# Kernel optimization log

Measured on AMD Instinct MI355X. Metric: run time of the kernel, lower is better.

Reference implementation:

```python
import jax, jax.numpy as jnp
import numpy as np

D_MODEL = 1024
H = 16
D_K = D_MODEL // H


def setup_inputs() -> dict:
    key = jax.random.key(0)
    ks = jax.random.split(key, 10)
    B, S = 2, 2048
    s = 1.0 / np.sqrt(D_MODEL)
    x = jax.random.normal(ks[0], (B, S, D_MODEL), dtype=jnp.float32)
    mask = jax.random.randint(ks[1], (B, 1, S, S), 0, 2, dtype=jnp.int32)
    w_q = jax.random.normal(ks[2], (D_MODEL, D_MODEL), dtype=jnp.float32) * s
    b_q = jnp.zeros((D_MODEL,), dtype=jnp.float32)
    w_k = jax.random.normal(ks[3], (D_MODEL, D_MODEL), dtype=jnp.float32) * s
    b_k = jnp.zeros((D_MODEL,), dtype=jnp.float32)
    w_v = jax.random.normal(ks[4], (D_MODEL, D_MODEL), dtype=jnp.float32) * s
    b_v = jnp.zeros((D_MODEL,), dtype=jnp.float32)
    w_o = jax.random.normal(ks[5], (D_MODEL, D_MODEL), dtype=jnp.float32) * s
    b_o = jnp.zeros((D_MODEL,), dtype=jnp.float32)
    return {"x": x, "mask": mask, "w_q": w_q, "b_q": b_q, "w_k": w_k,
            "b_k": b_k, "w_v": w_v, "b_v": b_v, "w_o": w_o, "b_o": b_o}


def reference(x, mask, w_q, b_q, w_k, b_k, w_v, b_v, w_o, b_o):
    B, S, _ = x.shape
    # projections; weights stored as (in, out) equivalents of torch Linear
    q = (x @ w_q + b_q).reshape(B, S, H, D_K).transpose(0, 2, 1, 3)  # bhsd
    k = (x @ w_k + b_k).reshape(B, S, H, D_K).transpose(0, 2, 1, 3)
    v = (x @ w_v + b_v).reshape(B, S, H, D_K).transpose(0, 2, 1, 3)
    scores = jnp.einsum('bhqd,bhkd->bhqk', q, k) / jnp.sqrt(jnp.float32(D_K))
    scores = jnp.where(mask == 0, jnp.float32(-1e9), scores)
    attn = jax.nn.softmax(scores, axis=-1)  # dropout omitted (eval mode)
    out = jnp.einsum('bhqk,bhkd->bhqd', attn, v)
    out = out.transpose(0, 2, 1, 3).reshape(B, S, D_MODEL)
    return out @ w_o + b_o
```

## Files before the change

### kernel.cpp

```cpp
#include <hip/hip_runtime.h>
#include <hip/hip_bf16.h>
#include <stdint.h>

#define D_MODEL 1024
#define NH 16
#define DK 64
#define SEQ 2048
#define BATCH 2
#define NTOK (BATCH * SEQ)

typedef __bf16 bf16;
typedef float f32x4 __attribute__((ext_vector_type(4)));
typedef __bf16 bf16x8 __attribute__((ext_vector_type(8)));
typedef __bf16 bf16x4 __attribute__((ext_vector_type(4)));

#define QSCALE 0.18033687932432668f

__device__ __forceinline__ void gload_lds16(const void* g, void* l) {
  __builtin_amdgcn_global_load_lds(
      (const __attribute__((address_space(1))) void*)g,
      (__attribute__((address_space(3))) void*)l, 16, 0, 0);
}

__global__ void prep_kernel(const float* __restrict__ x, bf16* __restrict__ xb,
                            const float* __restrict__ wq, const float* __restrict__ wk,
                            const float* __restrict__ wv, const float* __restrict__ wo,
                            bf16* __restrict__ wt,
                            const int* __restrict__ mask, unsigned long long* __restrict__ bits) {
  __shared__ float tile[32][33];
  const int bx = blockIdx.x;
  const int tid = threadIdx.x;
  if (bx < 4096) {
    int i = bx * 256 + tid;
    float4 v = reinterpret_cast<const float4*>(x)[i];
    bf16x4 o;
    o[0] = (bf16)v.x; o[1] = (bf16)v.y; o[2] = (bf16)v.z; o[3] = (bf16)v.w;
    reinterpret_cast<bf16x4*>(xb)[i] = o;
  } else if (bx < 8192) {
    int blk = bx - 4096;
    const int jt = blk & 127;
    const int kt = blk >> 7;
    const int tx = tid & 31, ty = tid >> 5;
    const int j0 = jt * 32;
    const int sel = j0 >> 10;
    const float* w = (sel == 0) ? wq : (sel == 1) ? wk : (sel == 2) ? wv : wo;
    const int jj0 = j0 & 1023;
#pragma unroll
    for (int i = 0; i < 4; ++i)
      tile[ty + i * 8][tx] = w[(size_t)(kt * 32 + ty + i * 8) * 1024 + jj0 + tx];
    __syncthreads();
#pragma unroll
    for (int i = 0; i < 4; ++i)
      wt[(size_t)(j0 + ty + i * 8) * 1024 + kt * 32 + tx] = (bf16)tile[tx][ty + i * 8];
  } else {
    int gt = (bx - 8192) * 256 + tid;
    int wid = gt >> 6;
    int l = gt & 63;
    int m = mask[(size_t)wid * 64 + l];
    unsigned long long b = __ballot(m != 0);
    if (l == 0) bits[wid] = b;
  }
}

__global__ __launch_bounds__(256) void gemm_qkv(
    const bf16* __restrict__ A, const bf16* __restrict__ Bt,
    const float* __restrict__ b0, const float* __restrict__ b1, const float* __restrict__ b2,
    bf16* __restrict__ out_q, bf16* __restrict__ out_k, bf16* __restrict__ out_vt) {
  __shared__ __align__(16) bf16 As[128 * 32];
  __shared__ __align__(16) bf16 Bs[128 * 32];
  const int tid = threadIdx.x;
  const int w = tid >> 6, l = tid & 63;
  const int wr = w >> 1, wc = w & 1;
  const int m0 = blockIdx.y * 128, n0 = blockIdx.x * 128;
  f32x4 acc[4][4] = {};
  const int lrow = l >> 2;
  const int lc8 = (l & 3) * 8;
  char* AsB = (char*)As;
  char* BsB = (char*)Bs;

  for (int k0 = 0; k0 < 1024; k0 += 32) {
#pragma unroll
    for (int is = 0; is < 2; ++is) {
      int arow = m0 + is * 64 + w * 16 + lrow;
      gload_lds16(A + (size_t)arow * 1024 + k0 + lc8, AsB + is * 4096 + w * 1024);
      int brow = n0 + is * 64 + w * 16 + lrow;
      gload_lds16(Bt + (size_t)brow * 1024 + k0 + lc8, BsB + is * 4096 + w * 1024);
    }
    __syncthreads();
    bf16x8 af[4], bfr[4];
#pragma unroll
    for (int m = 0; m < 4; ++m)
      af[m] = *reinterpret_cast<const bf16x8*>(As + (wr * 64 + m * 16 + (l & 15)) * 32 + (l >> 4) * 8);
#pragma unroll
    for (int n = 0; n < 4; ++n)
      bfr[n] = *reinterpret_cast<const bf16x8*>(Bs + (wc * 64 + n * 16 + (l & 15)) * 32 + (l >> 4) * 8);
#pragma unroll
    for (int m = 0; m < 4; ++m)
#pragma unroll
      for (int n = 0; n < 4; ++n)
        acc[m][n] = __builtin_amdgcn_mfma_f32_16x16x32_bf16(af[m], bfr[n], acc[m][n], 0, 0, 0);
    __syncthreads();
  }

#pragma unroll
  for (int m = 0; m < 4; ++m) {
    int ib = m0 + wr * 64 + m * 16 + 4 * (l >> 4);
#pragma unroll
    for (int n = 0; n < 4; ++n) {
      int j = n0 + wc * 64 + n * 16 + (l & 15);
      int sel = j >> 10, jj = j & 1023;
      const float* bp = (sel == 0) ? b0 : (sel == 1) ? b1 : b2;
      float bias = bp[jj];
      if (sel == 0) {
#pragma unroll
        for (int r = 0; r < 4; ++r)
          out_q[(size_t)(ib + r) * 1024 + jj] = (bf16)((acc[m][n][r] + bias) * QSCALE);
      } else if (sel == 1) {
#pragma unroll
        for (int r = 0; r < 4; ++r)
          out_k[(size_t)(ib + r) * 1024 + jj] = (bf16)(acc[m][n][r] + bias);
      } else {
        int hh = jj >> 6, dd = jj & 63;
        int bb = ib >> 11, ss = ib & 2047;
        bf16x4 v;
#pragma unroll
        for (int r = 0; r < 4; ++r) v[r] = (bf16)(acc[m][n][r] + bias);
        *reinterpret_cast<bf16x4*>(out_vt + ((size_t)(bb * NH + hh) * DK + dd) * SEQ + ss) = v;
      }
    }
  }
}

__global__ __launch_bounds__(256) void gemm_out(
    const bf16* __restrict__ A, const bf16* __restrict__ Bt,
    const float* __restrict__ bias, float* __restrict__ out) {
  __shared__ __align__(16) bf16 As[128 * 32];
  __shared__ __align__(16) bf16 Bs[64 * 32];
  const int tid = threadIdx.x;
  const int w = tid >> 6, l = tid & 63;
  const int wr = w >> 1, wc = w & 1;
  const int m0 = blockIdx.y * 128, n0 = blockIdx.x * 64;
  f32x4 acc[4][2] = {};
  const int lrow = l >> 2;
  const int lc8 = (l & 3) * 8;
  char* AsB = (char*)As;
  char* BsB = (char*)Bs;

  for (int k0 = 0; k0 < 1024; k0 += 32) {
#pragma unroll
    for (int is = 0; is < 2; ++is) {
      int arow = m0 + is * 64 + w * 16 + lrow;
      gload_lds16(A + (size_t)arow * 1024 + k0 + lc8, AsB + is * 4096 + w * 1024);
    }
    gload_lds16(Bt + (size_t)(n0 + w * 16 + lrow) * 1024 + k0 + lc8, BsB + w * 1024);
    __syncthreads();
    bf16x8 af[4], bfr[2];
#pragma unroll
    for (int m = 0; m < 4; ++m)
      af[m] = *reinterpret_cast<const bf16x8*>(As + (wr * 64 + m * 16 + (l & 15)) * 32 + (l >> 4) * 8);
#pragma unroll
    for (int n = 0; n < 2; ++n)
      bfr[n] = *reinterpret_cast<const bf16x8*>(Bs + (wc * 32 + n * 16 + (l & 15)) * 32 + (l >> 4) * 8);
#pragma unroll
    for (int m = 0; m < 4; ++m)
#pragma unroll
      for (int n = 0; n < 2; ++n)
        acc[m][n] = __builtin_amdgcn_mfma_f32_16x16x32_bf16(af[m], bfr[n], acc[m][n], 0, 0, 0);
    __syncthreads();
  }

#pragma unroll
  for (int m = 0; m < 4; ++m) {
    int ib = m0 + wr * 64 + m * 16 + 4 * (l >> 4);
#pragma unroll
    for (int n = 0; n < 2; ++n) {
      int j = n0 + wc * 32 + n * 16 + (l & 15);
      float bv = bias[j];
#pragma unroll
      for (int r = 0; r < 4; ++r)
        out[(size_t)(ib + r) * 1024 + j] = acc[m][n][r] + bv;
    }
  }
}

__global__ __launch_bounds__(256, 4) void attn_kernel(
    const bf16* __restrict__ qb, const bf16* __restrict__ kb,
    const bf16* __restrict__ vt, const unsigned long long* __restrict__ mbits,
    bf16* __restrict__ ob) {
  __shared__ __align__(16) bf16 Kbuf[2][64 * 64];
  __shared__ __align__(16) bf16 Vbuf[2][64 * 64];
  __shared__ __align__(16) bf16 Ps[4][16 * 64];
  const int tid = threadIdx.x;
  const int w = tid >> 6, l = tid & 63;
  const int qt = blockIdx.x, h = blockIdx.y, b = blockIdx.z;
  const int q0 = qt * 64;
  const int qrow = q0 + w * 16;
  const int tok0 = b * SEQ + qrow;

  bf16x8 qf[2];
#pragma unroll
  for (int kk = 0; kk < 2; ++kk)
    qf[kk] = *reinterpret_cast<const bf16x8*>(
        qb + (size_t)(tok0 + (l & 15)) * 1024 + h * 64 + kk * 32 + (l >> 4) * 8);

  float lsum[4] = {0.f, 0.f, 0.f, 0.f};
  f32x4 oacc[4] = {};

  const int swz = ((l & 7) ^ (l >> 3)) * 8;
  const bf16* ksrc = kb + (size_t)(b * SEQ) * 1024 + h * 64;
  const bf16* vsrc = vt + (size_t)(b * NH + h) * DK * SEQ;
  const unsigned long long* mrow = mbits + ((size_t)(b * SEQ + qrow + 4 * (l >> 4)) << 5);

  auto STAGE = [&](int buf, int kt) {
    char* KsB = (char*)Kbuf[buf];
    char* VsB = (char*)Vbuf[buf];
#pragma unroll
    for (int i = 0; i < 2; ++i) {
      int row = i * 32 + w * 8 + (l >> 3);
      gload_lds16(ksrc + (size_t)(kt * 64 + row) * 1024 + swz, KsB + i * 4096 + w * 1024);
      gload_lds16(vsrc + (size_t)row * SEQ + kt * 64 + swz, VsB + i * 4096 + w * 1024);
    }
  };

  STAGE(0, 0);
  for (int kt = 0; kt < 32; ++kt) {
    const int cur = kt & 1;
    unsigned long long mw[4];
#pragma unroll
    for (int r = 0; r < 4; ++r) mw[r] = mrow[(size_t)(r << 5) + kt];
    __builtin_amdgcn_sched_barrier(0);
    if (kt < 31) {
      STAGE(cur ^ 1, kt + 1);
      __builtin_amdgcn_sched_barrier(0);
      asm volatile("s_waitcnt vmcnt(8)" ::: "memory");
    } else {
      __builtin_amdgcn_sched_barrier(0);
      asm volatile("s_waitcnt vmcnt(4)" ::: "memory");
    }
    __builtin_amdgcn_s_barrier();
    __builtin_amdgcn_sched_barrier(0);

    const bf16* Ks = Kbuf[cur];
    const bf16* Vs = Vbuf[cur];

    f32x4 sa[4] = {};
#pragma unroll
    for (int kk = 0; kk < 2; ++kk) {
      bf16x8 kf[4];
      int c = kk * 4 + (l >> 4);
#pragma unroll
      for (int n = 0; n < 4; ++n) {
        int rr = n * 16 + (l & 15);
        kf[n] = *reinterpret_cast<const bf16x8*>(Ks + rr * 64 + ((c ^ (rr & 7)) << 3));
      }
#pragma unroll
      for (int n = 0; n < 4; ++n)
        sa[n] = __builtin_amdgcn_mfma_f32_16x16x32_bf16(qf[kk], kf[n], sa[n], 0, 0, 0);
    }

#pragma unroll
    for (int r = 0; r < 4; ++r) {
      int prow = 4 * (l >> 4) + r;
      unsigned long long sh = mw[r] >> (l & 15);
      unsigned int blo = (unsigned int)sh, bhi = (unsigned int)(sh >> 32);
      float p0 = (blo & 1u) ? __builtin_amdgcn_exp2f(sa[0][r]) : 0.f;
      float p1 = (blo & 0x10000u) ? __builtin_amdgcn_exp2f(sa[1][r]) : 0.f;
      float p2 = (bhi & 1u) ? __builtin_amdgcn_exp2f(sa[2][r]) : 0.f;
      float p3 = (bhi & 0x10000u) ? __builtin_amdgcn_exp2f(sa[3][r]) : 0.f;
      lsum[r] += (p0 + p1) + (p2 + p3);
      int colb = l & 7;
      int swzr = (prow & 7);
#pragma unroll
      for (int n = 0; n < 4; ++n) {
        int col = n * 16 + (l & 15);
        float p = (n == 0) ? p0 : (n == 1) ? p1 : (n == 2) ? p2 : p3;
        Ps[w][prow * 64 + (((col >> 3) ^ swzr) << 3) + colb] = (bf16)p;
      }
    }

#pragma unroll
    for (int kk = 0; kk < 2; ++kk) {
      int c = kk * 4 + (l >> 4);
      bf16x8 pa, vf[4];
      {
        int rr = l & 15;
        pa = *reinterpret_cast<const bf16x8*>(Ps[w] + rr * 64 + ((c ^ (rr & 7)) << 3));
      }
#pragma unroll
      for (int dn = 0; dn < 4; ++dn) {
        int rr = dn * 16 + (l & 15);
        vf[dn] = *reinterpret_cast<const bf16x8*>(Vs + rr * 64 + ((c ^ (rr & 7)) << 3));
      }
#pragma unroll
      for (int dn = 0; dn < 4; ++dn)
        oacc[dn] = __builtin_amdgcn_mfma_f32_16x16x32_bf16(pa, vf[dn], oacc[dn], 0, 0, 0);
    }
    __builtin_amdgcn_sched_barrier(0);
    __builtin_amdgcn_s_barrier();
  }

#pragma unroll
  for (int r = 0; r < 4; ++r) {
    float s = lsum[r];
    s += __shfl_xor(s, 1);
    s += __shfl_xor(s, 2);
    s += __shfl_xor(s, 4);
    s += __shfl_xor(s, 8);
    float inv = 1.f / s;
    int tok = tok0 + 4 * (l >> 4) + r;
#pragma unroll
    for (int dn = 0; dn < 4; ++dn)
      ob[(size_t)tok * 1024 + h * 64 + dn * 16 + (l & 15)] = (bf16)(oacc[dn][r] * inv);
  }
}

extern "C" void kernel_launch(void* const* d_in, const int* in_sizes, int n_in,
                              void* d_out, int out_size, void* d_ws, size_t ws_size,
                              hipStream_t stream) {
  const float* x = (const float*)d_in[0];
  const int* mask = (const int*)d_in[1];
  const float* wq = (const float*)d_in[2];
  const float* bq = (const float*)d_in[3];
  const float* wk = (const float*)d_in[4];
  const float* bk = (const float*)d_in[5];
  const float* wv = (const float*)d_in[6];
  const float* bv = (const float*)d_in[7];
  const float* wo = (const float*)d_in[8];
  const float* bo = (const float*)d_in[9];
  float* out = (float*)d_out;

  char* ws = (char*)d_ws;
  bf16* xb = (bf16*)(ws + (size_t)0);
  bf16* wt = (bf16*)(ws + ((size_t)8 << 20));
  bf16* qb = (bf16*)(ws + ((size_t)16 << 20));
  bf16* kb = (bf16*)(ws + ((size_t)24 << 20));
  bf16* vtb = (bf16*)(ws + ((size_t)32 << 20));
  bf16* ob = (bf16*)(ws + ((size_t)40 << 20));
  unsigned long long* mbits = (unsigned long long*)(ws + ((size_t)48 << 20));

  prep_kernel<<<40960, 256, 0, stream>>>(x, xb, wq, wk, wv, wo, wt, mask, mbits);
  gemm_qkv<<<dim3(24, 32), 256, 0, stream>>>(xb, wt, bq, bk, bv, qb, kb, vtb);
  attn_kernel<<<dim3(32, NH, BATCH), 256, 0, stream>>>(qb, kb, vtb, mbits, ob);
  gemm_out<<<dim3(16, 32), 256, 0, stream>>>(ob, wt + (size_t)3072 * 1024, bo, out);
}
```

Baseline: 242.0 us.

## Double-buffer GEMM loads, swizzle block order, transpose score MFMA in attention

Both projection GEMMs now double-buffer their LDS tiles and use explicit vmcnt waits with raw barriers, so global-to-LDS loads overlap the MFMA work of the previous k-step. All three kernels remap block indices so that groups of consecutive blocks share operand tiles, aiming for better L2 reuse. The attention kernel computes K·Q^T instead of Q·K^T, so each lane owns one query row: it needs one mask word per row instead of four, keeps a single running sum, and writes P to LDS as packed bf16 pairs. The row-sum normalisation gains a clamp against zero, and the doubled LDS in the GEMMs may lower occupancy.

Result: faster. 234.4 us (-3.1%).

```diff
diff --git a/kernel.cpp b/kernel.cpp
--- a/kernel.cpp
+++ b/kernel.cpp
@@ -13,6 +13,7 @@
 typedef float f32x4 __attribute__((ext_vector_type(4)));
 typedef __bf16 bf16x8 __attribute__((ext_vector_type(8)));
 typedef __bf16 bf16x4 __attribute__((ext_vector_type(4)));
+typedef __bf16 bf16x2 __attribute__((ext_vector_type(2)));
 
 #define QSCALE 0.18033687932432668f
 
@@ -66,19 +67,21 @@
     const bf16* __restrict__ A, const bf16* __restrict__ Bt,
     const float* __restrict__ b0, const float* __restrict__ b1, const float* __restrict__ b2,
     bf16* __restrict__ out_q, bf16* __restrict__ out_k, bf16* __restrict__ out_vt) {
-  __shared__ __align__(16) bf16 As[128 * 32];
-  __shared__ __align__(16) bf16 Bs[128 * 32];
+  __shared__ __align__(16) bf16 As[2][128 * 32];
+  __shared__ __align__(16) bf16 Bs[2][128 * 32];
   const int tid = threadIdx.x;
   const int w = tid >> 6, l = tid & 63;
   const int wr = w >> 1, wc = w & 1;
-  const int m0 = blockIdx.y * 128, n0 = blockIdx.x * 128;
+  int lin = blockIdx.x + 24 * blockIdx.y;
+  int nl = (lin & 7) * 96 + (lin >> 3);
+  const int m0 = (nl / 24) * 128, n0 = (nl % 24) * 128;
   f32x4 acc[4][4] = {};
   const int lrow = l >> 2;
   const int lc8 = (l & 3) * 8;
-  char* AsB = (char*)As;
-  char* BsB = (char*)Bs;
-
-  for (int k0 = 0; k0 < 1024; k0 += 32) {
+
+  auto STAGE = [&](int buf, int k0) {
+    char* AsB = (char*)As[buf];
+    char* BsB = (char*)Bs[buf];
 #pragma unroll
     for (int is = 0; is < 2; ++is) {
       int arow = m0 + is * 64 + w * 16 + lrow;
@@ -86,20 +89,37 @@
       int brow = n0 + is * 64 + w * 16 + lrow;
       gload_lds16(Bt + (size_t)brow * 1024 + k0 + lc8, BsB + is * 4096 + w * 1024);
     }
-    __syncthreads();
+  };
+
+  STAGE(0, 0);
+  for (int it = 0; it < 32; ++it) {
+    const int cur = it & 1;
+    if (it < 31) {
+      STAGE(cur ^ 1, (it + 1) * 32);
+      __builtin_amdgcn_sched_barrier(0);
+      asm volatile("s_waitcnt vmcnt(4)" ::: "memory");
+    } else {
+      __builtin_amdgcn_sched_barrier(0);
+      asm volatile("s_waitcnt vmcnt(0)" ::: "memory");
+    }
+    __builtin_amdgcn_s_barrier();
+    __builtin_amdgcn_sched_barrier(0);
+    const bf16* Asc = As[cur];
+    const bf16* Bsc = Bs[cur];
     bf16x8 af[4], bfr[4];
 #pragma unroll
     for (int m = 0; m < 4; ++m)
-      af[m] = *reinterpret_cast<const bf16x8*>(As + (wr * 64 + m * 16 + (l & 15)) * 32 + (l >> 4) * 8);
+      af[m] = *reinterpret_cast<const bf16x8*>(Asc + (wr * 64 + m * 16 + (l & 15)) * 32 + (l >> 4) * 8);
 #pragma unroll
     for (int n = 0; n < 4; ++n)
-      bfr[n] = *reinterpret_cast<const bf16x8*>(Bs + (wc * 64 + n * 16 + (l & 15)) * 32 + (l >> 4) * 8);
+      bfr[n] = *reinterpret_cast<const bf16x8*>(Bsc + (wc * 64 + n * 16 + (l & 15)) * 32 + (l >> 4) * 8);
 #pragma unroll
     for (int m = 0; m < 4; ++m)
 #pragma unroll
       for (int n = 0; n < 4; ++n)
         acc[m][n] = __builtin_amdgcn_mfma_f32_16x16x32_bf16(af[m], bfr[n], acc[m][n], 0, 0, 0);
-    __syncthreads();
+    __builtin_amdgcn_sched_barrier(0);
+    __builtin_amdgcn_s_barrier();
   }
 
 #pragma unroll
@@ -134,39 +154,58 @@
 __global__ __launch_bounds__(256) void gemm_out(
     const bf16* __restrict__ A, const bf16* __restrict__ Bt,
     const float* __restrict__ bias, float* __restrict__ out) {
-  __shared__ __align__(16) bf16 As[128 * 32];
-  __shared__ __align__(16) bf16 Bs[64 * 32];
+  __shared__ __align__(16) bf16 As[2][128 * 32];
+  __shared__ __align__(16) bf16 Bs[2][64 * 32];
   const int tid = threadIdx.x;
   const int w = tid >> 6, l = tid & 63;
   const int wr = w >> 1, wc = w & 1;
-  const int m0 = blockIdx.y * 128, n0 = blockIdx.x * 64;
+  int lin = blockIdx.x + 16 * blockIdx.y;
+  int nl = (lin & 7) * 64 + (lin >> 3);
+  const int m0 = (nl >> 4) * 128, n0 = (nl & 15) * 64;
   f32x4 acc[4][2] = {};
   const int lrow = l >> 2;
   const int lc8 = (l & 3) * 8;
-  char* AsB = (char*)As;
-  char* BsB = (char*)Bs;
-
-  for (int k0 = 0; k0 < 1024; k0 += 32) {
+
+  auto STAGE = [&](int buf, int k0) {
+    char* AsB = (char*)As[buf];
+    char* BsB = (char*)Bs[buf];
 #pragma unroll
     for (int is = 0; is < 2; ++is) {
       int arow = m0 + is * 64 + w * 16 + lrow;
       gload_lds16(A + (size_t)arow * 1024 + k0 + lc8, AsB + is * 4096 + w * 1024);
     }
     gload_lds16(Bt + (size_t)(n0 + w * 16 + lrow) * 1024 + k0 + lc8, BsB + w * 1024);
-    __syncthreads();
+  };
+
+  STAGE(0, 0);
+  for (int it = 0; it < 32; ++it) {
+    const int cur = it & 1;
+    if (it < 31) {
+      STAGE(cur ^ 1, (it + 1) * 32);
+      __builtin_amdgcn_sched_barrier(0);
+      asm volatile("s_waitcnt vmcnt(3)" ::: "memory");
+    } else {
+      __builtin_amdgcn_sched_barrier(0);
+      asm volatile("s_waitcnt vmcnt(0)" ::: "memory");
+    }
+    __builtin_amdgcn_s_barrier();
+    __builtin_amdgcn_sched_barrier(0);
+    const bf16* Asc = As[cur];
+    const bf16* Bsc = Bs[cur];
     bf16x8 af[4], bfr[2];
 #pragma unroll
     for (int m = 0; m < 4; ++m)
-      af[m] = *reinterpret_cast<const bf16x8*>(As + (wr * 64 + m * 16 + (l & 15)) * 32 + (l >> 4) * 8);
+      af[m] = *reinterpret_cast<const bf16x8*>(Asc + (wr * 64 + m * 16 + (l & 15)) * 32 + (l >> 4) * 8);
 #pragma unroll
     for (int n = 0; n < 2; ++n)
-      bfr[n] = *reinterpret_cast<const bf16x8*>(Bs + (wc * 32 + n * 16 + (l & 15)) * 32 + (l >> 4) * 8);
+      bfr[n] = *reinterpret_cast<const bf16x8*>(Bsc + (wc * 32 + n * 16 + (l & 15)) * 32 + (l >> 4) * 8);
 #pragma unroll
     for (int m = 0; m < 4; ++m)
 #pragma unroll
       for (int n = 0; n < 2; ++n)
         acc[m][n] = __builtin_amdgcn_mfma_f32_16x16x32_bf16(af[m], bfr[n], acc[m][n], 0, 0, 0);
-    __syncthreads();
+    __builtin_amdgcn_sched_barrier(0);
+    __builtin_amdgcn_s_barrier();
   }
 
 #pragma unroll
@@ -192,24 +231,27 @@
   __shared__ __align__(16) bf16 Ps[4][16 * 64];
   const int tid = threadIdx.x;
   const int w = tid >> 6, l = tid & 63;
-  const int qt = blockIdx.x, h = blockIdx.y, b = blockIdx.z;
+  int lin = blockIdx.x + 32 * blockIdx.y + 512 * blockIdx.z;
+  int nl = (lin & 7) * 128 + (lin >> 3);
+  const int qt = nl & 31, h = (nl >> 5) & 15, b = nl >> 9;
   const int q0 = qt * 64;
   const int qrow = q0 + w * 16;
   const int tok0 = b * SEQ + qrow;
+  const int a = l >> 4, c = l & 15;
 
   bf16x8 qf[2];
 #pragma unroll
   for (int kk = 0; kk < 2; ++kk)
     qf[kk] = *reinterpret_cast<const bf16x8*>(
-        qb + (size_t)(tok0 + (l & 15)) * 1024 + h * 64 + kk * 32 + (l >> 4) * 8);
-
-  float lsum[4] = {0.f, 0.f, 0.f, 0.f};
+        qb + (size_t)(tok0 + c) * 1024 + h * 64 + kk * 32 + a * 8);
+
+  float lsum = 0.f;
   f32x4 oacc[4] = {};
 
   const int swz = ((l & 7) ^ (l >> 3)) * 8;
   const bf16* ksrc = kb + (size_t)(b * SEQ) * 1024 + h * 64;
   const bf16* vsrc = vt + (size_t)(b * NH + h) * DK * SEQ;
-  const unsigned long long* mrow = mbits + ((size_t)(b * SEQ + qrow + 4 * (l >> 4)) << 5);
+  const unsigned long long* mrow = mbits + ((size_t)(b * SEQ + qrow + c) << 5);
 
   auto STAGE = [&](int buf, int kt) {
     char* KsB = (char*)Kbuf[buf];
@@ -225,9 +267,7 @@
   STAGE(0, 0);
   for (int kt = 0; kt < 32; ++kt) {
     const int cur = kt & 1;
-    unsigned long long mw[4];
-#pragma unroll
-    for (int r = 0; r < 4; ++r) mw[r] = mrow[(size_t)(r << 5) + kt];
+    unsigned long long mw = mrow[kt];
     __builtin_amdgcn_sched_barrier(0);
     if (kt < 31) {
       STAGE(cur ^ 1, kt + 1);
@@ -235,7 +275,7 @@
       asm volatile("s_waitcnt vmcnt(8)" ::: "memory");
     } else {
       __builtin_amdgcn_sched_barrier(0);
-      asm volatile("s_waitcnt vmcnt(4)" ::: "memory");
+      asm volatile("s_waitcnt vmcnt(0)" ::: "memory");
     }
     __builtin_amdgcn_s_barrier();
     __builtin_amdgcn_sched_barrier(0);
@@ -247,49 +287,45 @@
 #pragma unroll
     for (int kk = 0; kk < 2; ++kk) {
       bf16x8 kf[4];
-      int c = kk * 4 + (l >> 4);
+      int cc = kk * 4 + a;
 #pragma unroll
       for (int n = 0; n < 4; ++n) {
-        int rr = n * 16 + (l & 15);
-        kf[n] = *reinterpret_cast<const bf16x8*>(Ks + rr * 64 + ((c ^ (rr & 7)) << 3));
+        int rr = n * 16 + c;
+        kf[n] = *reinterpret_cast<const bf16x8*>(Ks + rr * 64 + ((cc ^ (rr & 7)) << 3));
       }
 #pragma unroll
       for (int n = 0; n < 4; ++n)
-        sa[n] = __builtin_amdgcn_mfma_f32_16x16x32_bf16(qf[kk], kf[n], sa[n], 0, 0, 0);
-    }
-
-#pragma unroll
-    for (int r = 0; r < 4; ++r) {
-      int prow = 4 * (l >> 4) + r;
-      unsigned long long sh = mw[r] >> (l & 15);
-      unsigned int blo = (unsigned int)sh, bhi = (unsigned int)(sh >> 32);
-      float p0 = (blo & 1u) ? __builtin_amdgcn_exp2f(sa[0][r]) : 0.f;
-      float p1 = (blo & 0x10000u) ? __builtin_amdgcn_exp2f(sa[1][r]) : 0.f;
-      float p2 = (bhi & 1u) ? __builtin_amdgcn_exp2f(sa[2][r]) : 0.f;
-      float p3 = (bhi & 0x10000u) ? __builtin_amdgcn_exp2f(sa[3][r]) : 0.f;
-      lsum[r] += (p0 + p1) + (p2 + p3);
-      int colb = l & 7;
-      int swzr = (prow & 7);
-#pragma unroll
-      for (int n = 0; n < 4; ++n) {
-        int col = n * 16 + (l & 15);
-        float p = (n == 0) ? p0 : (n == 1) ? p1 : (n == 2) ? p2 : p3;
-        Ps[w][prow * 64 + (((col >> 3) ^ swzr) << 3) + colb] = (bf16)p;
-      }
-    }
+        sa[n] = __builtin_amdgcn_mfma_f32_16x16x32_bf16(kf[n], qf[kk], sa[n], 0, 0, 0);
+    }
+
+    unsigned long long base = mw >> (a * 4);
+    float ps[4][4];
+#pragma unroll
+    for (int n = 0; n < 4; ++n)
+#pragma unroll
+      for (int r = 0; r < 4; ++r) {
+        bool on = (base >> (16 * n + r)) & 1ull;
+        float p = on ? __builtin_amdgcn_exp2f(sa[n][r]) : 0.f;
+        ps[n][r] = p;
+        lsum += p;
+      }
+#pragma unroll
+    for (int n = 0; n < 4; ++n)
+#pragma unroll
+      for (int pp = 0; pp < 2; ++pp) {
+        int chunk = (2 * n + (a >> 1)) ^ (c & 7);
+        bf16x2 v2 = {(bf16)ps[n][2 * pp], (bf16)ps[n][2 * pp + 1]};
+        *reinterpret_cast<bf16x2*>(Ps[w] + c * 64 + chunk * 8 + 4 * (a & 1) + 2 * pp) = v2;
+      }
 
 #pragma unroll
     for (int kk = 0; kk < 2; ++kk) {
-      int c = kk * 4 + (l >> 4);
-      bf16x8 pa, vf[4];
-      {
-        int rr = l & 15;
-        pa = *reinterpret_cast<const bf16x8*>(Ps[w] + rr * 64 + ((c ^ (rr & 7)) << 3));
-      }
+      bf16x8 pa = *reinterpret_cast<const bf16x8*>(Ps[w] + c * 64 + (((a + 4 * kk) ^ (c & 7)) << 3));
+      bf16x8 vf[4];
 #pragma unroll
       for (int dn = 0; dn < 4; ++dn) {
-        int rr = dn * 16 + (l & 15);
-        vf[dn] = *reinterpret_cast<const bf16x8*>(Vs + rr * 64 + ((c ^ (rr & 7)) << 3));
+        int rr = dn * 16 + c;
+        vf[dn] = *reinterpret_cast<const bf16x8*>(Vs + rr * 64 + (((kk * 4 + a) ^ (rr & 7)) << 3));
       }
 #pragma unroll
       for (int dn = 0; dn < 4; ++dn)
@@ -299,18 +335,17 @@
     __builtin_amdgcn_s_barrier();
   }
 
+  float s = lsum;
+  s += __shfl_xor(s, 16);
+  s += __shfl_xor(s, 32);
 #pragma unroll
   for (int r = 0; r < 4; ++r) {
-    float s = lsum[r];
-    s += __shfl_xor(s, 1);
-    s += __shfl_xor(s, 2);
-    s += __shfl_xor(s, 4);
-    s += __shfl_xor(s, 8);
-    float inv = 1.f / s;
-    int tok = tok0 + 4 * (l >> 4) + r;
+    float sr = __shfl(s, 4 * a + r);
+    float inv = 1.f / fmaxf(sr, 1e-35f);
+    int tok = tok0 + 4 * a + r;
 #pragma unroll
     for (int dn = 0; dn < 4; ++dn)
-      ob[(size_t)tok * 1024 + h * 64 + dn * 16 + (l & 15)] = (bf16)(oacc[dn][r] * inv);
+      ob[(size_t)tok * 1024 + h * 64 + dn * 16 + c] = (bf16)(oacc[dn][r] * inv);
   }
 }
 
```
